# Performance work log

Hardware: AMD Instinct MI355X
Metric: run time of the kernel (lower is better)

Reference implementation:

```python
import jax, jax.numpy as jnp
import numpy as np

B, L, HID = 2, 2048, 2048
NH, NKV, HD = 16, 4, 128
LAT = 512
Q_PER_KV = NH // NKV
SCALE = HD ** -0.5
ROPE_THETA = 10000.0


def setup_inputs() -> dict:
    key = jax.random.key(0)
    ks = jax.random.split(key, 6)
    s = lambda fan_in: 1.0 / np.sqrt(fan_in)
    return {
        "x": jax.random.normal(ks[0], (B, L, HID), dtype=jnp.float32),
        "Wq": jax.random.normal(ks[1], (HID, NH * HD), dtype=jnp.float32) * s(HID),
        "Wc": jax.random.normal(ks[2], (HID, LAT), dtype=jnp.float32) * s(HID),
        "Wk": jax.random.normal(ks[3], (LAT, NKV * HD), dtype=jnp.float32) * s(LAT),
        "Wv": jax.random.normal(ks[4], (LAT, NKV * HD), dtype=jnp.float32) * s(LAT),
        "Wo": jax.random.normal(ks[5], (NH * HD, HID), dtype=jnp.float32) * s(NH * HD),
        "attention_mask": jnp.ones((B, L), dtype=jnp.int32),
    }


def _rope(t):  # t: [B, H, L, HD]
    half = HD // 2
    inv_freq = 1.0 / (ROPE_THETA ** (jnp.arange(half, dtype=jnp.float32) / half))
    pos = jnp.arange(t.shape[2], dtype=jnp.float32)
    freqs = pos[:, None] * inv_freq[None, :]          # [L, half]
    cos = jnp.cos(freqs)[None, None].astype(t.dtype)  # [1,1,L,half]
    sin = jnp.sin(freqs)[None, None].astype(t.dtype)
    t1, t2 = t[..., :half], t[..., half:]
    return jnp.concatenate([t1 * cos - t2 * sin, t2 * cos + t1 * sin], axis=-1)


def reference(x, Wq, Wc, Wk, Wv, Wo, attention_mask):
    q = (x @ Wq).reshape(B, L, NH, HD).transpose(0, 2, 1, 3)      # [B,NH,L,HD]
    c = x @ Wc                                                    # latent bottleneck
    k = (c @ Wk).reshape(B, L, NKV, HD).transpose(0, 2, 1, 3)     # [B,NKV,L,HD]
    v = (c @ Wv).reshape(B, L, NKV, HD).transpose(0, 2, 1, 3)
    # GQA repeat_interleave along head axis
    k = jnp.repeat(k, Q_PER_KV, axis=1)                           # [B,NH,L,HD]
    v = jnp.repeat(v, Q_PER_KV, axis=1)
    q = _rope(q)
    k = _rope(k)
    att = jnp.einsum("bhqd,bhkd->bhqk", q, k) * SCALE             # [B,NH,L,L]
    neg = jnp.finfo(att.dtype).min
    causal = jnp.tril(jnp.ones((L, L), dtype=bool))[None, None]
    att = jnp.where(causal, att, neg)
    key_mask = (attention_mask > 0)[:, None, None, :]             # [B,1,1,L]
    att = jnp.where(key_mask, att, neg)
    att = jax.nn.softmax(att, axis=-1)
    y = jnp.einsum("bhqk,bhkd->bhqd", att, v)
    y = y.transpose(0, 2, 1, 3).reshape(B, L, NH * HD)
    return y @ Wo
```

## Files before the change

### kernel.cpp

```cpp
#include <hip/hip_runtime.h>
#include <hip/hip_bf16.h>
#include <cstdint>
#include <cstddef>

#define B_    2
#define L_    2048
#define HID_  2048
#define NH_   16
#define NKV_  4
#define HD_   128
#define LAT_  512
#define SCALE_ 0.08838834764831845f
#define SC2_   0.1275174365f

typedef unsigned short u16;
typedef unsigned int   u32;
typedef __attribute__((ext_vector_type(8))) short   short8;
typedef __attribute__((ext_vector_type(4))) float   floatx4;

typedef __attribute__((address_space(1))) const u32 gas_u32;
typedef __attribute__((address_space(3))) u32       las_u32;

__device__ __forceinline__ void gl_lds16(const u16* g, u16* l) {
    __builtin_amdgcn_global_load_lds((gas_u32*)g, (las_u32*)l, 16, 0, 0);
}

__device__ __forceinline__ float bf2f(u16 u) {
    union { u32 i; float f; } v; v.i = ((u32)u) << 16; return v.f;
}
__device__ __forceinline__ u16 f2bf(float f) {
    union { float f; u32 u; } v; v.f = f;
    u32 u = v.u;
    u32 r = (u + 0x7fffu + ((u >> 16) & 1u)) >> 16;
    return (u16)r;
}
__device__ __forceinline__ u16 f2bf_hw(float f) {
    union { __hip_bfloat16 h; u16 u; } c;
    c.h = __float2bfloat16(f);
    return c.u;
}

__global__ void cvt_kernel(const float* __restrict__ in, u16* __restrict__ out, int n4) {
    int i = blockIdx.x * 256 + threadIdx.x;
    if (i < n4) {
        float4 v = ((const float4*)in)[i];
        union { u16 w[4]; uint2 v; } o;
        o.w[0] = f2bf(v.x); o.w[1] = f2bf(v.y);
        o.w[2] = f2bf(v.z); o.w[3] = f2bf(v.w);
        ((uint2*)out)[i] = o.v;
    }
}

__global__ void cvt_transpose_kernel(const float* __restrict__ in, u16* __restrict__ out,
                                     int R, int C) {
    __shared__ u16 tile[32][33];
    int c0 = blockIdx.x * 32, r0 = blockIdx.y * 32;
    int tx = threadIdx.x & 31, ty = threadIdx.x >> 5;
    for (int i = ty; i < 32; i += 8)
        tile[tx][i] = f2bf(in[(size_t)(r0 + i) * C + c0 + tx]);
    __syncthreads();
    for (int i = ty; i < 32; i += 8)
        out[(size_t)(c0 + i) * R + r0 + tx] = tile[i][tx];
}

__global__ void transpose_v_kernel(const u16* __restrict__ in, u16* __restrict__ out) {
    __shared__ u16 t[32][33];
    int lt = blockIdx.x, dt = blockIdx.y, bh = blockIdx.z;
    int b = bh >> 2, kvh = bh & 3;
    int tx = threadIdx.x & 31, ty = threadIdx.x >> 5;
    for (int i = ty; i < 32; i += 8)
        t[i][tx] = in[(((size_t)b * L_ + lt * 32 + i) * NKV_ + kvh) * HD_ + dt * 32 + tx];
    __syncthreads();
    const int lcol = lt * 32 + tx;
    const int k6 = lcol & 63;
    const int ni = k6 >> 4, qd = (k6 >> 2) & 3, r = k6 & 3;
    const int p = ((ni >> 1) << 5) | (qd << 3) | ((ni & 1) << 2) | r;
    const int csig = (lcol & ~63) | p;
    for (int i = ty; i < 32; i += 8)
        out[((size_t)bh * HD_ + dt * 32 + i) * L_ + csig] = t[tx][i];
}

template<int OUT_BF16>
__global__ __launch_bounds__(256)
void gemm_bt(const u16* __restrict__ A, const u16* __restrict__ BT,
             void* __restrict__ C, int M, int N, int K) {
    __shared__ __align__(16) u16 As[128][32];
    __shared__ __align__(16) u16 Bs[128][32];
    const int tid  = threadIdx.x;
    const int m0   = blockIdx.y * 128, n0 = blockIdx.x * 128;
    const int wave = tid >> 6, lane = tid & 63;
    const int wm   = (wave >> 1) * 64, wn = (wave & 1) * 64;
    const int quad = lane >> 4, l16 = lane & 15;

    const int srow = wave * 32 + (lane >> 2);
    const int scol = (lane & 3) * 8;
    const u16* aptr0 = A  + (size_t)(m0 + srow) * K + scol;
    const u16* bptr0 = BT + (size_t)(n0 + srow) * K + scol;
    const u16* aptr1 = aptr0 + (size_t)16 * K;
    const u16* bptr1 = bptr0 + (size_t)16 * K;
    u16* lA0 = &As[wave * 32][0];
    u16* lA1 = &As[wave * 32 + 16][0];
    u16* lB0 = &Bs[wave * 32][0];
    u16* lB1 = &Bs[wave * 32 + 16][0];

    floatx4 acc[4][4] = {};

    for (int k0 = 0; k0 < K; k0 += 32) {
        gl_lds16(aptr0 + k0, lA0);
        gl_lds16(aptr1 + k0, lA1);
        gl_lds16(bptr0 + k0, lB0);
        gl_lds16(bptr1 + k0, lB1);
        __syncthreads();

        short8 af[4], bfr[4];
        #pragma unroll
        for (int i = 0; i < 4; i++) af[i]  = *(const short8*)&As[wm + i * 16 + l16][quad * 8];
        #pragma unroll
        for (int i = 0; i < 4; i++) bfr[i] = *(const short8*)&Bs[wn + i * 16 + l16][quad * 8];
        #pragma unroll
        for (int mi = 0; mi < 4; mi++)
            #pragma unroll
            for (int ni = 0; ni < 4; ni++)
                acc[mi][ni] = __builtin_amdgcn_mfma_f32_16x16x32_bf16(
                    af[mi], bfr[ni], acc[mi][ni], 0, 0, 0);
        __syncthreads();
    }

    #pragma unroll
    for (int mi = 0; mi < 4; mi++) {
        #pragma unroll
        for (int ni = 0; ni < 4; ni++) {
            #pragma unroll
            for (int r = 0; r < 4; r++) {
                int row = m0 + wm + mi * 16 + quad * 4 + r;
                int col = n0 + wn + ni * 16 + l16;
                float v = acc[mi][ni][r];
                if (OUT_BF16) ((u16*)C)[(size_t)row * N + col] = f2bf(v);
                else          ((float*)C)[(size_t)row * N + col] = v;
            }
        }
    }
}

__global__ __launch_bounds__(256)
void gemm_bt_split(const u16* __restrict__ A, const u16* __restrict__ BT,
                   u16* __restrict__ C0, u16* __restrict__ C1,
                   int M, int N, int K, int Nsplit, int N0, int N1) {
    __shared__ __align__(16) u16 As[128][32];
    __shared__ __align__(16) u16 Bs[128][32];
    const int tid  = threadIdx.x;
    const int m0   = blockIdx.y * 128, n0 = blockIdx.x * 128;
    const int wave = tid >> 6, lane = tid & 63;
    const int wm   = (wave >> 1) * 64, wn = (wave & 1) * 64;
    const int quad = lane >> 4, l16 = lane & 15;

    const int srow = wave * 32 + (lane >> 2);
    const int scol = (lane & 3) * 8;
    const u16* aptr0 = A  + (size_t)(m0 + srow) * K + scol;
    const u16* bptr0 = BT + (size_t)(n0 + srow) * K + scol;
    const u16* aptr1 = aptr0 + (size_t)16 * K;
    const u16* bptr1 = bptr0 + (size_t)16 * K;
    u16* lA0 = &As[wave * 32][0];
    u16* lA1 = &As[wave * 32 + 16][0];
    u16* lB0 = &Bs[wave * 32][0];
    u16* lB1 = &Bs[wave * 32 + 16][0];

    floatx4 acc[4][4] = {};

    for (int k0 = 0; k0 < K; k0 += 32) {
        gl_lds16(aptr0 + k0, lA0);
        gl_lds16(aptr1 + k0, lA1);
        gl_lds16(bptr0 + k0, lB0);
        gl_lds16(bptr1 + k0, lB1);
        __syncthreads();

        short8 af[4], bfr[4];
        #pragma unroll
        for (int i = 0; i < 4; i++) af[i]  = *(const short8*)&As[wm + i * 16 + l16][quad * 8];
        #pragma unroll
        for (int i = 0; i < 4; i++) bfr[i] = *(const short8*)&Bs[wn + i * 16 + l16][quad * 8];
        #pragma unroll
        for (int mi = 0; mi < 4; mi++)
            #pragma unroll
            for (int ni = 0; ni < 4; ni++)
                acc[mi][ni] = __builtin_amdgcn_mfma_f32_16x16x32_bf16(
                    af[mi], bfr[ni], acc[mi][ni], 0, 0, 0);
        __syncthreads();
    }

    const int side = (n0 >= Nsplit);
    u16* Cw = side ? C1 : C0;
    const int nw = side ? N1 : N0;
    const int cbase = side ? Nsplit : 0;

    #pragma unroll
    for (int mi = 0; mi < 4; mi++) {
        #pragma unroll
        for (int ni = 0; ni < 4; ni++) {
            #pragma unroll
            for (int r = 0; r < 4; r++) {
                int row = m0 + wm + mi * 16 + quad * 4 + r;
                int col = n0 + wn + ni * 16 + l16 - cbase;
                Cw[(size_t)row * nw + col] = f2bf(acc[mi][ni][r]);
            }
        }
    }
}

__global__ void rope_perm(const u16* __restrict__ in, u16* __restrict__ out,
                          int nh, int nhbits) {
    int idx = blockIdx.x * 256 + threadIdx.x;
    int d = idx & 63;
    int l = (idx >> 6) & (L_ - 1);
    int h = (idx >> 17) & (nh - 1);
    int b = idx >> (17 + nhbits);
    const u16* src = &in[(((size_t)b * L_ + l) * nh + h) * HD_];
    u16* dst = &out[(((size_t)b * nh + h) * L_ + l) * HD_];
    float t1 = bf2f(src[d]), t2 = bf2f(src[d + 64]);
    float inv = expf(-(float)d * 0.14391156831212787f);
    float fr = (float)l * inv;
    float c = cosf(fr), sn = sinf(fr);
    dst[d]      = f2bf(t1 * c - t2 * sn);
    dst[d + 64] = f2bf(t2 * c + t1 * sn);
}

__global__ __launch_bounds__(256)
void attn_mfma(const u16* __restrict__ Q, const u16* __restrict__ K,
               const u16* __restrict__ Vt, const int* __restrict__ amask,
               u16* __restrict__ Y, float* __restrict__ Opart,
               float* __restrict__ lpart) {
    __shared__ __align__(16) u16 Ks[64][128];
    __shared__ __align__(16) u16 Vs[128][64];

    const int tid  = threadIdx.x;
    const int wave = tid >> 6, lane = tid & 63;
    const int quad = lane >> 4, l16 = lane & 15;

    const int bid = blockIdx.x;
    const int s   = bid >> 8;
    const int c   = bid & 255;
    const int bkvh = c & 7;
    const int j   = c >> 3;
    const int b   = bkvh >> 2, kvh = bkvh & 3;

    const int H  = ((32 + j) >> 1) + 1;
    const int Lg = ((31 - j) >> 1) + 1;
    const int m2 = max((H + 1) >> 1, (Lg + 1) >> 1);
    const int m3 = max((H + 2) / 3, Lg);
    const int nh = (m2 <= m3) ? 2 : 3;
    const int nl = 4 - nh;
    int t, kt0, kt1, pi;
    if (s < nh) {
        t = 32 + j; kt0 = (H * s) / nh; kt1 = (H * (s + 1)) / nh; pi = bid;
    } else {
        t = 31 - j;
        const int ls = s - nh;
        kt0 = (Lg * ls) / nl; kt1 = (Lg * (ls + 1)) / nl;
        pi = (nl == 1) ? -1 : bid;
    }

    const int h   = kvh * 4 + wave;
    const int q0  = t * 32;

    const u16* Qbase = Q  + ((size_t)b * NH_  + h)   * L_ * HD_;
    const u16* Kbase = K  + ((size_t)b * NKV_ + kvh) * L_ * HD_;
    const u16* Vbase = Vt + ((size_t)b * NKV_ + kvh) * (size_t)HD_ * L_;
    const int* mbase = amask + b * L_;

    short8 qa[2][4];
    #pragma unroll
    for (int mi = 0; mi < 2; ++mi)
        #pragma unroll
        for (int ks = 0; ks < 4; ++ks)
            qa[mi][ks] = *(const short8*)&Qbase[(size_t)(q0 + mi * 16 + l16) * HD_ + ks * 32 + quad * 8];

    floatx4 Oacc[2][8] = {};
    float lsum[2] = {0.0f, 0.0f};

    const int slK = lane & 15, rKl = lane >> 4;
    const int slV = lane & 7,  rVl = lane >> 3;
    int okg[4], ovg[4];
    u16 *klds[4], *vlds[4];
    #pragma unroll
    for (int cc = 0; cc < 4; ++cc) {
        const int seg = wave * 4 + cc;
        const int rk = seg * 4 + rKl;
        okg[cc] = rk * HD_ + ((slK ^ (rk & 7)) * 8);
        klds[cc] = (u16*)Ks + seg * 512;
        const int rv = seg * 8 + rVl;
        ovg[cc] = rv * L_ + ((slV ^ (rv & 7)) * 8);
        vlds[cc] = (u16*)Vs + seg * 512;
    }
    const u16* kgb = Kbase + (size_t)kt0 * 64 * HD_;
    const u16* vgb = Vbase + kt0 * 64;

    for (int kt = kt0; kt < kt1; ++kt) {
        const int kbase = kt * 64;

        #pragma unroll
        for (int cc = 0; cc < 4; ++cc) {
            gl_lds16(kgb + okg[cc], klds[cc]);
            gl_lds16(vgb + ovg[cc], vlds[cc]);
        }
        const int am_l = mbase[kbase + lane];
        const bool allm = __all(am_l > 0);
        kgb += (size_t)64 * HD_;
        vgb += 64;
        __syncthreads();

        floatx4 sfr[2][4] = {};
        __builtin_amdgcn_s_setprio(1);
        #pragma unroll
        for (int ni = 0; ni < 4; ++ni) {
            #pragma unroll
            for (int ks = 0; ks < 4; ++ks) {
                short8 kf = *(const short8*)&Ks[ni * 16 + l16][((ks * 4 + quad) ^ (l16 & 7)) * 8];
                sfr[0][ni] = __builtin_amdgcn_mfma_f32_16x16x32_bf16(kf, qa[0][ks], sfr[0][ni], 0, 0, 0);
                sfr[1][ni] = __builtin_amdgcn_mfma_f32_16x16x32_bf16(kf, qa[1][ks], sfr[1][ni], 0, 0, 0);
            }
        }
        __builtin_amdgcn_s_setprio(0);

        if (allm & (kbase + 63 <= q0)) {
            #pragma unroll
            for (int mi = 0; mi < 2; ++mi)
                #pragma unroll
                for (int ni = 0; ni < 4; ++ni)
                    #pragma unroll
                    for (int r = 0; r < 4; ++r) {
                        float p = exp2f(fmaf(sfr[mi][ni][r], SC2_, -8.0f));
                        lsum[mi] += p;
                        sfr[mi][ni][r] = p;
                    }
        } else {
            #pragma unroll
            for (int ni = 0; ni < 4; ++ni) {
                const int4 amv = *(const int4*)&mbase[kbase + ni * 16 + quad * 4];
                const int amr[4] = {amv.x, amv.y, amv.z, amv.w};
                #pragma unroll
                for (int mi = 0; mi < 2; ++mi) {
                    const int qrow = q0 + mi * 16 + l16;
                    #pragma unroll
                    for (int r = 0; r < 4; ++r) {
                        const int kpos = kbase + ni * 16 + quad * 4 + r;
                        const bool ok = (kpos <= qrow) & (amr[r] > 0);
                        float p = ok ? exp2f(fmaf(sfr[mi][ni][r], SC2_, -8.0f)) : 0.0f;
                        lsum[mi] += p;
                        sfr[mi][ni][r] = p;
                    }
                }
            }
        }

        short8 pf[2][2];
        #pragma unroll
        for (int mi = 0; mi < 2; ++mi)
            #pragma unroll
            for (int kc = 0; kc < 2; ++kc) {
                union { u16 w[8]; short8 s8; } u;
                #pragma unroll
                for (int r = 0; r < 4; ++r) {
                    u.w[r]     = f2bf_hw(sfr[mi][kc * 2][r]);
                    u.w[4 + r] = f2bf_hw(sfr[mi][kc * 2 + 1][r]);
                }
                pf[mi][kc] = u.s8;
            }

        __builtin_amdgcn_s_setprio(1);
        #pragma unroll
        for (int kc = 0; kc < 2; ++kc) {
            #pragma unroll
            for (int dn = 0; dn < 8; ++dn) {
                short8 vf = *(const short8*)&Vs[dn * 16 + l16][((kc * 4 + quad) ^ (l16 & 7)) * 8];
                Oacc[0][dn] = __builtin_amdgcn_mfma_f32_16x16x32_bf16(pf[0][kc], vf, Oacc[0][dn], 0, 0, 0);
                Oacc[1][dn] = __builtin_amdgcn_mfma_f32_16x16x32_bf16(pf[1][kc], vf, Oacc[1][dn], 0, 0, 0);
            }
        }
        __builtin_amdgcn_s_setprio(0);
        __syncthreads();
    }

    float lr[2];
    #pragma unroll
    for (int mi = 0; mi < 2; ++mi) {
        float v = lsum[mi];
        v += __shfl_xor(v, 16);
        v += __shfl_xor(v, 32);
        lr[mi] = v;
    }

    if (pi < 0) {
        #pragma unroll
        for (int mi = 0; mi < 2; ++mi) {
            #pragma unroll
            for (int r = 0; r < 4; ++r) {
                const float linv = 1.0f / __shfl(lr[mi], quad * 4 + r);
                const int qrow = q0 + mi * 16 + quad * 4 + r;
                u16* dst = &Y[(((size_t)b * L_ + qrow) * NH_ + h) * HD_];
                #pragma unroll
                for (int dn = 0; dn < 8; ++dn)
                    dst[dn * 16 + l16] = f2bf(Oacc[mi][dn][r] * linv);
            }
        }
    } else {
        float* od = Opart + ((size_t)pi * 4 + wave) * 32 * 128;
        float* lp = lpart + ((size_t)pi * 4 + wave) * 32;
        #pragma unroll
        for (int mi = 0; mi < 2; ++mi) {
            if (quad == 0)
                __builtin_nontemporal_store(lr[mi], &lp[mi * 16 + l16]);
            #pragma unroll
            for (int r = 0; r < 4; ++r) {
                const int qi = mi * 16 + quad * 4 + r;
                #pragma unroll
                for (int dn = 0; dn < 8; ++dn)
                    __builtin_nontemporal_store(Oacc[mi][dn][r],
                                                &od[(size_t)qi * 128 + dn * 16 + l16]);
            }
        }
    }
}

__global__ __launch_bounds__(256)
void attn_combine(const float* __restrict__ Opart, const float* __restrict__ lpart,
                  u16* __restrict__ Y) {
    const int cb = blockIdx.x;
    const int c  = cb & 255, z = cb >> 8;
    const int tile = z >> 2, hw = z & 3;
    const int bkvh = c & 7, j = c >> 3;
    const int b = bkvh >> 2, kvh = bkvh & 3;
    const int h = kvh * 4 + hw;
    const int H  = ((32 + j) >> 1) + 1;
    const int Lg = ((31 - j) >> 1) + 1;
    const int m2 = max((H + 1) >> 1, (Lg + 1) >> 1);
    const int m3 = max((H + 2) / 3, Lg);
    const int nh = (m2 <= m3) ? 2 : 3;
    const int nl = 4 - nh;
    if (tile == 1 && nl == 1) return;
    const int s0 = tile ? nh : 0;
    const int ns = tile ? nl : nh;
    const int t  = tile ? (31 - j) : (32 + j);
    const int tid = threadIdx.x;
    const int q = tid >> 3, dg = tid & 7;

    float4 a0 = {0,0,0,0}, a1 = {0,0,0,0}, a2 = {0,0,0,0}, a3 = {0,0,0,0};
    float lacc = 0.0f;
    for (int i = 0; i < ns; ++i) {
        const size_t rowb = ((size_t)((s0 + i) * 256 + c) * 4 + hw) * 32 + q;
        lacc += lpart[rowb];
        const float4* op = (const float4*)(Opart + rowb * 128 + dg * 16);
        float4 v0 = op[0], v1 = op[1], v2 = op[2], v3 = op[3];
        a0.x += v0.x; a0.y += v0.y; a0.z += v0.z; a0.w += v0.w;
        a1.x += v1.x; a1.y += v1.y; a1.z += v1.z; a1.w += v1.w;
        a2.x += v2.x; a2.y += v2.y; a2.z += v2.z; a2.w += v2.w;
        a3.x += v3.x; a3.y += v3.y; a3.z += v3.z; a3.w += v3.w;
    }
    const float linv = 1.0f / lacc;
    const int qrow = t * 32 + q;
    u16* dst = &Y[(((size_t)b * L_ + qrow) * NH_ + h) * HD_ + dg * 16];

    u16 tmp[16];
    tmp[0]  = f2bf(a0.x * linv); tmp[1]  = f2bf(a0.y * linv);
    tmp[2]  = f2bf(a0.z * linv); tmp[3]  = f2bf(a0.w * linv);
    tmp[4]  = f2bf(a1.x * linv); tmp[5]  = f2bf(a1.y * linv);
    tmp[6]  = f2bf(a1.z * linv); tmp[7]  = f2bf(a1.w * linv);
    tmp[8]  = f2bf(a2.x * linv); tmp[9]  = f2bf(a2.y * linv);
    tmp[10] = f2bf(a2.z * linv); tmp[11] = f2bf(a2.w * linv);
    tmp[12] = f2bf(a3.x * linv); tmp[13] = f2bf(a3.y * linv);
    tmp[14] = f2bf(a3.z * linv); tmp[15] = f2bf(a3.w * linv);
    *(uint4*)(dst)     = *(const uint4*)(&tmp[0]);
    *(uint4*)(dst + 8) = *(const uint4*)(&tmp[8]);
}

extern "C" void kernel_launch(void* const* d_in, const int* in_sizes, int n_in,
                              void* d_out, int out_size, void* d_ws, size_t ws_size,
                              hipStream_t stream) {
    const float* x  = (const float*)d_in[0];
    const float* Wq = (const float*)d_in[1];
    const float* Wc = (const float*)d_in[2];
    const float* Wk = (const float*)d_in[3];
    const float* Wv = (const float*)d_in[4];
    const float* Wo = (const float*)d_in[5];
    const int* amask = (const int*)d_in[6];
    float* out = (float*)d_out;

    char* p = (char*)d_ws;
    auto alloc = [&](size_t elems) {
        u16* r = (u16*)p;
        p += ((elems * 2 + 255) / 256) * 256;
        return r;
    };
    u16* WoT  = alloc((size_t)2048 * 2048);
    u16* qbuf = alloc((size_t)4096 * 2048);
    u16* Qr   = alloc((size_t)4096 * 2048);
    u16* Kr   = alloc((size_t)4096 * 512);
    u16* Vt   = alloc((size_t)4096 * 512);
    char* pdead = p;
    u16* Xb   = alloc((size_t)4096 * 2048);
    u16* WqT  = alloc((size_t)2048 * 2048);
    u16* WcT  = alloc((size_t)512 * 2048);
    u16* WkT  = alloc((size_t)512 * 512);
    u16* WvT  = alloc((size_t)512 * 512);
    u16* cbuf = alloc((size_t)4096 * 512);
    u16* kbuf = alloc((size_t)4096 * 512);
    u16* vbuf = alloc((size_t)4096 * 512);
    float* Opart = (float*)pdead;
    float* lpart = (float*)(pdead + (size_t)1024 * 4 * 32 * 128 * 4);

    cvt_kernel<<<8388608 / 4 / 256, 256, 0, stream>>>(x, Xb, 8388608 / 4);
    cvt_transpose_kernel<<<dim3(2048 / 32, 2048 / 32), 256, 0, stream>>>(Wq, WqT, 2048, 2048);
    cvt_transpose_kernel<<<dim3(512 / 32, 2048 / 32), 256, 0, stream>>>(Wc, WcT, 2048, 512);
    cvt_transpose_kernel<<<dim3(512 / 32, 512 / 32), 256, 0, stream>>>(Wk, WkT, 512, 512);
    cvt_transpose_kernel<<<dim3(512 / 32, 512 / 32), 256, 0, stream>>>(Wv, WvT, 512, 512);
    cvt_transpose_kernel<<<dim3(2048 / 32, 2048 / 32), 256, 0, stream>>>(Wo, WoT, 2048, 2048);

    gemm_bt_split<<<dim3(20, 32), 256, 0, stream>>>(Xb, WqT, qbuf, cbuf,
                                                    4096, 2560, 2048, 2048, 2048, 512);
    gemm_bt_split<<<dim3(8, 32), 256, 0, stream>>>(cbuf, WkT, kbuf, vbuf,
                                                   4096, 1024, 512, 512, 512, 512);

    rope_perm<<<(2 * 16 * 2048 * 64) / 256, 256, 0, stream>>>(qbuf, Qr, 16, 4);
    rope_perm<<<(2 * 4 * 2048 * 64) / 256, 256, 0, stream>>>(kbuf, Kr, 4, 2);
    transpose_v_kernel<<<dim3(64, 4, 8), 256, 0, stream>>>(vbuf, Vt);

    attn_mfma<<<dim3(1024), 256, 0, stream>>>(Qr, Kr, Vt, amask, qbuf, Opart, lpart);
    attn_combine<<<dim3(2048), 256, 0, stream>>>(Opart, lpart, qbuf);

    gemm_bt<0><<<dim3(16, 32), 256, 0, stream>>>(qbuf, WoT, out, 4096, 2048, 2048);
}
```

Baseline: 359.5 us.

## Fold latent Wc·Wk/Wv into one weight, double GEMM K-tile with swizzled LDS

Precomputes the combined weight (Wc@[Wk|Wv])^T with a small GEMM, so K and V come straight out of the main x GEMM. This removes the separate latent c GEMM and its intermediate buffer. The GEMM kernels now stage 64-wide K tiles with an XOR-swizzled LDS layout, which halves the barrier count and avoids bank conflicts. Weight conversion launches are batched into fewer kernels. The cost is a wider main GEMM (3072 instead of 2560 columns) and bf16 rounding of the fused weight, which changes numerics slightly.

```diff
diff --git a/kernel.cpp b/kernel.cpp
--- a/kernel.cpp
+++ b/kernel.cpp
@@ -51,9 +51,12 @@
     }
 }
 
-__global__ void cvt_transpose_kernel(const float* __restrict__ in, u16* __restrict__ out,
-                                     int R, int C) {
+__global__ void cvt_transpose2_kernel(const float* __restrict__ in0, u16* __restrict__ out0,
+                                      const float* __restrict__ in1, u16* __restrict__ out1,
+                                      int R, int C) {
     __shared__ u16 tile[32][33];
+    const float* in = blockIdx.z ? in1 : in0;
+    u16* out = blockIdx.z ? out1 : out0;
     int c0 = blockIdx.x * 32, r0 = blockIdx.y * 32;
     int tx = threadIdx.x & 31, ty = threadIdx.x >> 5;
     for (int i = ty; i < 32; i += 8)
@@ -63,13 +66,13 @@
         out[(size_t)(c0 + i) * R + r0 + tx] = tile[i][tx];
 }
 
-__global__ void transpose_v_kernel(const u16* __restrict__ in, u16* __restrict__ out) {
+__global__ void transpose_v_kernel(const u16* __restrict__ kv, u16* __restrict__ out) {
     __shared__ u16 t[32][33];
     int lt = blockIdx.x, dt = blockIdx.y, bh = blockIdx.z;
     int b = bh >> 2, kvh = bh & 3;
     int tx = threadIdx.x & 31, ty = threadIdx.x >> 5;
     for (int i = ty; i < 32; i += 8)
-        t[i][tx] = in[(((size_t)b * L_ + lt * 32 + i) * NKV_ + kvh) * HD_ + dt * 32 + tx];
+        t[i][tx] = kv[(size_t)(b * L_ + lt * 32 + i) * 1024 + 512 + kvh * HD_ + dt * 32 + tx];
     __syncthreads();
     const int lcol = lt * 32 + tx;
     const int k6 = lcol & 63;
@@ -84,45 +87,55 @@
 __global__ __launch_bounds__(256)
 void gemm_bt(const u16* __restrict__ A, const u16* __restrict__ BT,
              void* __restrict__ C, int M, int N, int K) {
-    __shared__ __align__(16) u16 As[128][32];
-    __shared__ __align__(16) u16 Bs[128][32];
+    __shared__ __align__(16) u16 As[128][64];
+    __shared__ __align__(16) u16 Bs[128][64];
     const int tid  = threadIdx.x;
     const int m0   = blockIdx.y * 128, n0 = blockIdx.x * 128;
     const int wave = tid >> 6, lane = tid & 63;
     const int wm   = (wave >> 1) * 64, wn = (wave & 1) * 64;
     const int quad = lane >> 4, l16 = lane & 15;
 
-    const int srow = wave * 32 + (lane >> 2);
-    const int scol = (lane & 3) * 8;
-    const u16* aptr0 = A  + (size_t)(m0 + srow) * K + scol;
-    const u16* bptr0 = BT + (size_t)(n0 + srow) * K + scol;
-    const u16* aptr1 = aptr0 + (size_t)16 * K;
-    const u16* bptr1 = bptr0 + (size_t)16 * K;
-    u16* lA0 = &As[wave * 32][0];
-    u16* lA1 = &As[wave * 32 + 16][0];
-    u16* lB0 = &Bs[wave * 32][0];
-    u16* lB1 = &Bs[wave * 32 + 16][0];
+    const int r8 = lane >> 3, srcc = ((lane & 7) ^ r8) * 8;
+    const u16* ap[4]; const u16* bp[4];
+    u16 *la[4], *lb[4];
+    #pragma unroll
+    for (int cc = 0; cc < 4; ++cc) {
+        const int seg = wave * 4 + cc;
+        const int row = seg * 8 + r8;
+        ap[cc] = A  + (size_t)(m0 + row) * K + srcc;
+        bp[cc] = BT + (size_t)(n0 + row) * K + srcc;
+        la[cc] = &As[0][0] + seg * 512;
+        lb[cc] = &Bs[0][0] + seg * 512;
+    }
 
     floatx4 acc[4][4] = {};
 
-    for (int k0 = 0; k0 < K; k0 += 32) {
-        gl_lds16(aptr0 + k0, lA0);
-        gl_lds16(aptr1 + k0, lA1);
-        gl_lds16(bptr0 + k0, lB0);
-        gl_lds16(bptr1 + k0, lB1);
+    for (int k0 = 0; k0 < K; k0 += 64) {
+        #pragma unroll
+        for (int cc = 0; cc < 4; ++cc) {
+            gl_lds16(ap[cc] + k0, la[cc]);
+            gl_lds16(bp[cc] + k0, lb[cc]);
+        }
         __syncthreads();
 
-        short8 af[4], bfr[4];
-        #pragma unroll
-        for (int i = 0; i < 4; i++) af[i]  = *(const short8*)&As[wm + i * 16 + l16][quad * 8];
-        #pragma unroll
-        for (int i = 0; i < 4; i++) bfr[i] = *(const short8*)&Bs[wn + i * 16 + l16][quad * 8];
-        #pragma unroll
-        for (int mi = 0; mi < 4; mi++)
-            #pragma unroll
-            for (int ni = 0; ni < 4; ni++)
-                acc[mi][ni] = __builtin_amdgcn_mfma_f32_16x16x32_bf16(
-                    af[mi], bfr[ni], acc[mi][ni], 0, 0, 0);
+        short8 af[4][2], bfr[4][2];
+        #pragma unroll
+        for (int i = 0; i < 4; i++) {
+            const int ra = wm + i * 16 + l16, rb = wn + i * 16 + l16;
+            #pragma unroll
+            for (int kk = 0; kk < 2; kk++) {
+                af[i][kk]  = *(const short8*)&As[ra][((kk * 4 + quad) ^ (l16 & 7)) * 8];
+                bfr[i][kk] = *(const short8*)&Bs[rb][((kk * 4 + quad) ^ (l16 & 7)) * 8];
+            }
+        }
+        #pragma unroll
+        for (int kk = 0; kk < 2; kk++)
+            #pragma unroll
+            for (int mi = 0; mi < 4; mi++)
+                #pragma unroll
+                for (int ni = 0; ni < 4; ni++)
+                    acc[mi][ni] = __builtin_amdgcn_mfma_f32_16x16x32_bf16(
+                        af[mi][kk], bfr[ni][kk], acc[mi][ni], 0, 0, 0);
         __syncthreads();
     }
 
@@ -146,45 +159,55 @@
 void gemm_bt_split(const u16* __restrict__ A, const u16* __restrict__ BT,
                    u16* __restrict__ C0, u16* __restrict__ C1,
                    int M, int N, int K, int Nsplit, int N0, int N1) {
-    __shared__ __align__(16) u16 As[128][32];
-    __shared__ __align__(16) u16 Bs[128][32];
+    __shared__ __align__(16) u16 As[128][64];
+    __shared__ __align__(16) u16 Bs[128][64];
     const int tid  = threadIdx.x;
     const int m0   = blockIdx.y * 128, n0 = blockIdx.x * 128;
     const int wave = tid >> 6, lane = tid & 63;
     const int wm   = (wave >> 1) * 64, wn = (wave & 1) * 64;
     const int quad = lane >> 4, l16 = lane & 15;
 
-    const int srow = wave * 32 + (lane >> 2);
-    const int scol = (lane & 3) * 8;
-    const u16* aptr0 = A  + (size_t)(m0 + srow) * K + scol;
-    const u16* bptr0 = BT + (size_t)(n0 + srow) * K + scol;
-    const u16* aptr1 = aptr0 + (size_t)16 * K;
-    const u16* bptr1 = bptr0 + (size_t)16 * K;
-    u16* lA0 = &As[wave * 32][0];
-    u16* lA1 = &As[wave * 32 + 16][0];
-    u16* lB0 = &Bs[wave * 32][0];
-    u16* lB1 = &Bs[wave * 32 + 16][0];
+    const int r8 = lane >> 3, srcc = ((lane & 7) ^ r8) * 8;
+    const u16* ap[4]; const u16* bp[4];
+    u16 *la[4], *lb[4];
+    #pragma unroll
+    for (int cc = 0; cc < 4; ++cc) {
+        const int seg = wave * 4 + cc;
+        const int row = seg * 8 + r8;
+        ap[cc] = A  + (size_t)(m0 + row) * K + srcc;
+        bp[cc] = BT + (size_t)(n0 + row) * K + srcc;
+        la[cc] = &As[0][0] + seg * 512;
+        lb[cc] = &Bs[0][0] + seg * 512;
+    }
 
     floatx4 acc[4][4] = {};
 
-    for (int k0 = 0; k0 < K; k0 += 32) {
-        gl_lds16(aptr0 + k0, lA0);
-        gl_lds16(aptr1 + k0, lA1);
-        gl_lds16(bptr0 + k0, lB0);
-        gl_lds16(bptr1 + k0, lB1);
+    for (int k0 = 0; k0 < K; k0 += 64) {
+        #pragma unroll
+        for (int cc = 0; cc < 4; ++cc) {
+            gl_lds16(ap[cc] + k0, la[cc]);
+            gl_lds16(bp[cc] + k0, lb[cc]);
+        }
         __syncthreads();
 
-        short8 af[4], bfr[4];
-        #pragma unroll
-        for (int i = 0; i < 4; i++) af[i]  = *(const short8*)&As[wm + i * 16 + l16][quad * 8];
-        #pragma unroll
-        for (int i = 0; i < 4; i++) bfr[i] = *(const short8*)&Bs[wn + i * 16 + l16][quad * 8];
-        #pragma unroll
-        for (int mi = 0; mi < 4; mi++)
-            #pragma unroll
-            for (int ni = 0; ni < 4; ni++)
-                acc[mi][ni] = __builtin_amdgcn_mfma_f32_16x16x32_bf16(
-                    af[mi], bfr[ni], acc[mi][ni], 0, 0, 0);
+        short8 af[4][2], bfr[4][2];
+        #pragma unroll
+        for (int i = 0; i < 4; i++) {
+            const int ra = wm + i * 16 + l16, rb = wn + i * 16 + l16;
+            #pragma unroll
+            for (int kk = 0; kk < 2; kk++) {
+                af[i][kk]  = *(const short8*)&As[ra][((kk * 4 + quad) ^ (l16 & 7)) * 8];
+                bfr[i][kk] = *(const short8*)&Bs[rb][((kk * 4 + quad) ^ (l16 & 7)) * 8];
+            }
+        }
+        #pragma unroll
+        for (int kk = 0; kk < 2; kk++)
+            #pragma unroll
+            for (int mi = 0; mi < 4; mi++)
+                #pragma unroll
+                for (int ni = 0; ni < 4; ni++)
+                    acc[mi][ni] = __builtin_amdgcn_mfma_f32_16x16x32_bf16(
+                        af[mi][kk], bfr[ni][kk], acc[mi][ni], 0, 0, 0);
         __syncthreads();
     }
 
@@ -208,13 +231,13 @@
 }
 
 __global__ void rope_perm(const u16* __restrict__ in, u16* __restrict__ out,
-                          int nh, int nhbits) {
+                          int nh, int nhbits, int rs) {
     int idx = blockIdx.x * 256 + threadIdx.x;
     int d = idx & 63;
     int l = (idx >> 6) & (L_ - 1);
     int h = (idx >> 17) & (nh - 1);
     int b = idx >> (17 + nhbits);
-    const u16* src = &in[(((size_t)b * L_ + l) * nh + h) * HD_];
+    const u16* src = &in[(size_t)(b * L_ + l) * rs + h * HD_];
     u16* dst = &out[(((size_t)b * nh + h) * L_ + l) * HD_];
     float t1 = bf2f(src[d]), t2 = bf2f(src[d + 64]);
     float inv = expf(-(float)d * 0.14391156831212787f);
@@ -496,32 +519,29 @@
     u16* Kr   = alloc((size_t)4096 * 512);
     u16* Vt   = alloc((size_t)4096 * 512);
     char* pdead = p;
-    u16* Xb   = alloc((size_t)4096 * 2048);
     u16* WqT  = alloc((size_t)2048 * 2048);
-    u16* WcT  = alloc((size_t)512 * 2048);
+    u16* WckvT= alloc((size_t)1024 * 2048);
     u16* WkT  = alloc((size_t)512 * 512);
     u16* WvT  = alloc((size_t)512 * 512);
-    u16* cbuf = alloc((size_t)4096 * 512);
-    u16* kbuf = alloc((size_t)4096 * 512);
-    u16* vbuf = alloc((size_t)4096 * 512);
+    u16* Wcb  = alloc((size_t)2048 * 512);
+    u16* Xb   = alloc((size_t)4096 * 2048);
+    u16* kvbuf= alloc((size_t)4096 * 1024);
     float* Opart = (float*)pdead;
     float* lpart = (float*)(pdead + (size_t)1024 * 4 * 32 * 128 * 4);
 
     cvt_kernel<<<8388608 / 4 / 256, 256, 0, stream>>>(x, Xb, 8388608 / 4);
-    cvt_transpose_kernel<<<dim3(2048 / 32, 2048 / 32), 256, 0, stream>>>(Wq, WqT, 2048, 2048);
-    cvt_transpose_kernel<<<dim3(512 / 32, 2048 / 32), 256, 0, stream>>>(Wc, WcT, 2048, 512);
-    cvt_transpose_kernel<<<dim3(512 / 32, 512 / 32), 256, 0, stream>>>(Wk, WkT, 512, 512);
-    cvt_transpose_kernel<<<dim3(512 / 32, 512 / 32), 256, 0, stream>>>(Wv, WvT, 512, 512);
-    cvt_transpose_kernel<<<dim3(2048 / 32, 2048 / 32), 256, 0, stream>>>(Wo, WoT, 2048, 2048);
-
-    gemm_bt_split<<<dim3(20, 32), 256, 0, stream>>>(Xb, WqT, qbuf, cbuf,
-                                                    4096, 2560, 2048, 2048, 2048, 512);
-    gemm_bt_split<<<dim3(8, 32), 256, 0, stream>>>(cbuf, WkT, kbuf, vbuf,
-                                                   4096, 1024, 512, 512, 512, 512);
-
-    rope_perm<<<(2 * 16 * 2048 * 64) / 256, 256, 0, stream>>>(qbuf, Qr, 16, 4);
-    rope_perm<<<(2 * 4 * 2048 * 64) / 256, 256, 0, stream>>>(kbuf, Kr, 4, 2);
-    transpose_v_kernel<<<dim3(64, 4, 8), 256, 0, stream>>>(vbuf, Vt);
+    cvt_kernel<<<(2048 * 512 / 4) / 256, 256, 0, stream>>>(Wc, Wcb, 2048 * 512 / 4);
+    cvt_transpose2_kernel<<<dim3(64, 64, 2), 256, 0, stream>>>(Wq, WqT, Wo, WoT, 2048, 2048);
+    cvt_transpose2_kernel<<<dim3(16, 16, 2), 256, 0, stream>>>(Wk, WkT, Wv, WvT, 512, 512);
+
+    gemm_bt<1><<<dim3(16, 8), 256, 0, stream>>>(WkT, Wcb, WckvT, 1024, 2048, 512);
+
+    gemm_bt_split<<<dim3(24, 32), 256, 0, stream>>>(Xb, WqT, qbuf, kvbuf,
+                                                    4096, 3072, 2048, 2048, 2048, 1024);
+
+    rope_perm<<<(2 * 16 * 2048 * 64) / 256, 256, 0, stream>>>(qbuf, Qr, 16, 4, 2048);
+    rope_perm<<<(2 * 4 * 2048 * 64) / 256, 256, 0, stream>>>(kvbuf, Kr, 4, 2, 1024);
+    transpose_v_kernel<<<dim3(64, 4, 8), 256, 0, stream>>>(kvbuf, Vt);
 
     attn_mfma<<<dim3(1024), 256, 0, stream>>>(Qr, Kr, Vt, amask, qbuf, Opart, lpart);
     attn_combine<<<dim3(2048), 256, 0, stream>>>(Opart, lpart, qbuf);
```

New measurement: 350.3 us. 1.03x faster.
